# Kernel optimization log

Hardware: AMD Instinct MI355X
Metric: run time of the kernel (lower is better)

## Reference

```python
import jax, jax.numpy as jnp
import numpy as np

B, I, O, C, U = 32, 2048, 32, 16, 32  # batch, in_channels(caps), out_capsules, in_capsules(dim), unit_size
NUM_ITERS = 3


def setup_inputs() -> dict:
    key = jax.random.key(0)
    k1, k2 = jax.random.split(key)
    x = jax.random.normal(k1, (B, I, C), dtype=jnp.float32)
    w = jax.random.normal(k2, (I, O, C, U), dtype=jnp.float32)
    return {"x": x, "w": w}


def _squash(v):
    # faithful to original: vec * |vec| / (1 + |vec|^2), norm over last (unit) dim
    n = jnp.linalg.norm(v, axis=-1, keepdims=True)
    return v * n / (1.0 + n * n)


def reference(x, w):
    # u_hat[b,i,o,u] = sum_c x[b,i,c] * w[i,o,c,u]   (the original's x @ w with singleton dims dropped)
    u_hat = jnp.einsum('bic,iocu->biou', x, w)  # [B,I,O,U]
    b_log = jnp.zeros((I, O, 1), dtype=x.dtype)
    v = None
    for _ in range(NUM_ITERS):
        # original computes softmax over dim=2 of [I,O,1] (a singleton dim) -> all ones; kept faithful
        c = jax.nn.softmax(b_log, axis=2)[..., 0]  # [I,O]
        s = jnp.einsum('io,biou->bou', c, u_hat)   # sum over input capsules
        v = _squash(s)                              # [B,O,U]
        # agreement: per-(b,i,o) dot(u_hat, v), then mean over batch (original's update.mean(dim=0))
        agree = jnp.einsum('biou,bou->io', u_hat, v) / B
        b_log = b_log + agree[..., None]
    return v[:, :, None, :]  # matches original v.squeeze(1) -> [B, O, 1, U]
```

## Files before the change

### kernel.cpp

```cpp
#include <hip/hip_runtime.h>
#include <math.h>

#define B_   32
#define I_   2048
#define O_   32
#define C_   16
#define U_   32
#define NCOL (O_ * U_)
#define TI   4
#define NBLK (I_ / TI)
#define SLICE (B_ * NCOL)


__global__ __launch_bounds__(256, 2) void caps_partial(const float* __restrict__ x,
                                                       const float* __restrict__ w,
                                                       float* __restrict__ ws) {
    __shared__ float xs[TI * C_ * 33];
    const int tid = threadIdx.x;
    const int i0 = blockIdx.x * TI;

    for (int k = tid; k < B_ * TI * C_; k += 256) {
        int b   = k >> 6;
        int rem = k & 63;
        xs[rem * 33 + b] = x[(size_t)b * (I_ * C_) + (size_t)i0 * C_ + rem];
    }
    __syncthreads();

    const int o  = tid >> 3;
    const int u4 = (tid & 7) << 2;
    const float* wp = w + (size_t)i0 * (O_ * C_ * U_) + o * (C_ * U_) + u4;

    float4 acc[B_];
#pragma unroll
    for (int b = 0; b < B_; ++b) acc[b] = make_float4(0.f, 0.f, 0.f, 0.f);

    for (int il = 0; il < TI; ++il) {
        const float* wpi = wp + (size_t)il * (O_ * C_ * U_);
        const float* xr  = &xs[il * C_ * 33];
        float4 wv[C_];
#pragma unroll
        for (int c = 0; c < C_; ++c) wv[c] = *(const float4*)(wpi + c * U_);
#pragma unroll
        for (int c = 0; c < C_; ++c) {
            const float* xc = xr + c * 33;
#pragma unroll
            for (int b = 0; b < B_; ++b) {
                float xb = xc[b];
                acc[b].x = fmaf(xb, wv[c].x, acc[b].x);
                acc[b].y = fmaf(xb, wv[c].y, acc[b].y);
                acc[b].z = fmaf(xb, wv[c].z, acc[b].z);
                acc[b].w = fmaf(xb, wv[c].w, acc[b].w);
            }
        }
    }

    float* op = ws + (size_t)blockIdx.x * SLICE + u4 + o * U_;
#pragma unroll
    for (int b = 0; b < B_; ++b)
        *(float4*)(op + (size_t)b * NCOL) = acc[b];
}

__global__ void caps_reduce_squash(const float* __restrict__ ws,
                                   float* __restrict__ out) {
    int t = blockIdx.x * 256 + threadIdx.x;
    float s = 0.f;
#pragma unroll 8
    for (int p = 0; p < NBLK; ++p)
        s += ws[(size_t)p * SLICE + t];
    float ss = s * s;
    ss += __shfl_xor(ss, 1);
    ss += __shfl_xor(ss, 2);
    ss += __shfl_xor(ss, 4);
    ss += __shfl_xor(ss, 8);
    ss += __shfl_xor(ss, 16);
    float n = sqrtf(ss);
    out[t] = s * n / (1.0f + ss);
}

__global__ __launch_bounds__(256, 2) void caps_main_atomic(const float* __restrict__ x,
                                                           const float* __restrict__ w,
                                                           float* __restrict__ out) {
    __shared__ float xs[TI * C_ * 33];
    const int tid = threadIdx.x;
    const int i0 = blockIdx.x * TI;
    for (int k = tid; k < B_ * TI * C_; k += 256) {
        int b = k >> 6, rem = k & 63;
        xs[rem * 33 + b] = x[(size_t)b * (I_ * C_) + (size_t)i0 * C_ + rem];
    }
    __syncthreads();
    const int o = tid >> 3, u4 = (tid & 7) << 2;
    const float* wp = w + (size_t)i0 * (O_ * C_ * U_) + o * (C_ * U_) + u4;
    float4 acc[B_];
#pragma unroll
    for (int b = 0; b < B_; ++b) acc[b] = make_float4(0.f, 0.f, 0.f, 0.f);
    for (int il = 0; il < TI; ++il) {
        const float* wpi = wp + (size_t)il * (O_ * C_ * U_);
        const float* xr = &xs[il * C_ * 33];
#pragma unroll
        for (int c = 0; c < C_; ++c) {
            float4 wv = *(const float4*)(wpi + c * U_);
            const float* xc = xr + c * 33;
#pragma unroll
            for (int b = 0; b < B_; ++b) {
                float xb = xc[b];
                acc[b].x = fmaf(xb, wv.x, acc[b].x);
                acc[b].y = fmaf(xb, wv.y, acc[b].y);
                acc[b].z = fmaf(xb, wv.z, acc[b].z);
                acc[b].w = fmaf(xb, wv.w, acc[b].w);
            }
        }
    }
    float* op = out + o * U_ + u4;
#pragma unroll
    for (int b = 0; b < B_; ++b) {
        float* p = op + (size_t)b * NCOL;
        atomicAdd(p + 0, acc[b].x);
        atomicAdd(p + 1, acc[b].y);
        atomicAdd(p + 2, acc[b].z);
        atomicAdd(p + 3, acc[b].w);
    }
}

__global__ void caps_squash_inplace(float* __restrict__ out) {
    int t = blockIdx.x * 256 + threadIdx.x;
    float s = out[t];
    float ss = s * s;
    ss += __shfl_xor(ss, 1);
    ss += __shfl_xor(ss, 2);
    ss += __shfl_xor(ss, 4);
    ss += __shfl_xor(ss, 8);
    ss += __shfl_xor(ss, 16);
    float n = sqrtf(ss);
    out[t] = s * n / (1.0f + ss);
}

extern "C" void kernel_launch(void* const* d_in, const int* in_sizes, int n_in,
                              void* d_out, int out_size, void* d_ws, size_t ws_size,
                              hipStream_t stream) {
    const float* x = (const float*)d_in[0];
    const float* w = (const float*)d_in[1];
    float* out = (float*)d_out;

    const size_t need = (size_t)NBLK * SLICE * sizeof(float);
    if (ws_size >= need) {
        float* ws = (float*)d_ws;
        caps_partial<<<NBLK, 256, 0, stream>>>(x, w, ws);
        caps_reduce_squash<<<SLICE / 256, 256, 0, stream>>>(ws, out);
    } else {
        hipMemsetAsync(out, 0, (size_t)SLICE * sizeof(float), stream);
        caps_main_atomic<<<NBLK, 256, 0, stream>>>(x, w, out);
        caps_squash_inplace<<<SLICE / 256, 256, 0, stream>>>(out);
    }
}
```

Before: 223.7 us.

## Split batch across thread halves, vectorize LDS reads, parallelize reduction

The partial kernel now uses 512 threads per block, with each half handling 16 of the 32 batch rows. This halves the accumulator registers per thread so more waves can be resident. Shared-memory x reads become float4 loads with a padded stride of 36, and weights are loaded in groups of four channels instead of all sixteen at once. The reduce kernel splits the 512-partial sum between two thread halves and combines them through shared memory, giving twice as many threads to the memory-bound reduction. The cost is weight loads duplicated across the two halves and possible bank conflicts from the new padding.

After: 211.8 us. -5.4%, faster.

```diff
diff --git a/kernel.cpp b/kernel.cpp
--- a/kernel.cpp
+++ b/kernel.cpp
@@ -10,71 +10,101 @@
 #define TI   4
 #define NBLK (I_ / TI)
 #define SLICE (B_ * NCOL)
+#define BH   16
+#define XS   36
 
 
-__global__ __launch_bounds__(256, 2) void caps_partial(const float* __restrict__ x,
+__global__ __launch_bounds__(512, 4) void caps_partial(const float* __restrict__ x,
                                                        const float* __restrict__ w,
                                                        float* __restrict__ ws) {
-    __shared__ float xs[TI * C_ * 33];
+    __shared__ float xs[TI * C_ * XS];
     const int tid = threadIdx.x;
     const int i0 = blockIdx.x * TI;
 
-    for (int k = tid; k < B_ * TI * C_; k += 256) {
+    for (int k = tid; k < B_ * TI * C_; k += 512) {
         int b   = k >> 6;
         int rem = k & 63;
-        xs[rem * 33 + b] = x[(size_t)b * (I_ * C_) + (size_t)i0 * C_ + rem];
+        xs[rem * XS + b] = x[(size_t)b * (I_ * C_) + (size_t)i0 * C_ + rem];
     }
     __syncthreads();
 
-    const int o  = tid >> 3;
-    const int u4 = (tid & 7) << 2;
+    const int bh = tid >> 8;
+    const int ct = tid & 255;
+    const int o  = ct >> 3;
+    const int u4 = (ct & 7) << 2;
     const float* wp = w + (size_t)i0 * (O_ * C_ * U_) + o * (C_ * U_) + u4;
 
-    float4 acc[B_];
+    float4 acc[BH];
 #pragma unroll
-    for (int b = 0; b < B_; ++b) acc[b] = make_float4(0.f, 0.f, 0.f, 0.f);
+    for (int b = 0; b < BH; ++b) acc[b] = make_float4(0.f, 0.f, 0.f, 0.f);
 
     for (int il = 0; il < TI; ++il) {
         const float* wpi = wp + (size_t)il * (O_ * C_ * U_);
-        const float* xr  = &xs[il * C_ * 33];
-        float4 wv[C_];
+        const float* xr  = &xs[il * C_ * XS + bh * BH];
 #pragma unroll
-        for (int c = 0; c < C_; ++c) wv[c] = *(const float4*)(wpi + c * U_);
+        for (int cc = 0; cc < C_; cc += 4) {
+            float4 wv[4];
 #pragma unroll
-        for (int c = 0; c < C_; ++c) {
-            const float* xc = xr + c * 33;
+            for (int j = 0; j < 4; ++j)
+                wv[j] = *(const float4*)(wpi + (cc + j) * U_);
 #pragma unroll
-            for (int b = 0; b < B_; ++b) {
-                float xb = xc[b];
-                acc[b].x = fmaf(xb, wv[c].x, acc[b].x);
-                acc[b].y = fmaf(xb, wv[c].y, acc[b].y);
-                acc[b].z = fmaf(xb, wv[c].z, acc[b].z);
-                acc[b].w = fmaf(xb, wv[c].w, acc[b].w);
+            for (int j = 0; j < 4; ++j) {
+                const float4* xv = (const float4*)(xr + (cc + j) * XS);
+#pragma unroll
+                for (int q = 0; q < 4; ++q) {
+                    float4 xq = xv[q];
+                    float4* a = &acc[q * 4];
+                    a[0].x = fmaf(xq.x, wv[j].x, a[0].x);
+                    a[0].y = fmaf(xq.x, wv[j].y, a[0].y);
+                    a[0].z = fmaf(xq.x, wv[j].z, a[0].z);
+                    a[0].w = fmaf(xq.x, wv[j].w, a[0].w);
+                    a[1].x = fmaf(xq.y, wv[j].x, a[1].x);
+                    a[1].y = fmaf(xq.y, wv[j].y, a[1].y);
+                    a[1].z = fmaf(xq.y, wv[j].z, a[1].z);
+                    a[1].w = fmaf(xq.y, wv[j].w, a[1].w);
+                    a[2].x = fmaf(xq.z, wv[j].x, a[2].x);
+                    a[2].y = fmaf(xq.z, wv[j].y, a[2].y);
+                    a[2].z = fmaf(xq.z, wv[j].z, a[2].z);
+                    a[2].w = fmaf(xq.z, wv[j].w, a[2].w);
+                    a[3].x = fmaf(xq.w, wv[j].x, a[3].x);
+                    a[3].y = fmaf(xq.w, wv[j].y, a[3].y);
+                    a[3].z = fmaf(xq.w, wv[j].z, a[3].z);
+                    a[3].w = fmaf(xq.w, wv[j].w, a[3].w);
+                }
             }
         }
     }
 
-    float* op = ws + (size_t)blockIdx.x * SLICE + u4 + o * U_;
+    float* op = ws + (size_t)blockIdx.x * SLICE + (size_t)(bh * BH) * NCOL + o * U_ + u4;
 #pragma unroll
-    for (int b = 0; b < B_; ++b)
+    for (int b = 0; b < BH; ++b)
         *(float4*)(op + (size_t)b * NCOL) = acc[b];
 }
 
-__global__ void caps_reduce_squash(const float* __restrict__ ws,
-                                   float* __restrict__ out) {
-    int t = blockIdx.x * 256 + threadIdx.x;
+__global__ __launch_bounds__(256) void caps_reduce_squash(const float* __restrict__ ws,
+                                                          float* __restrict__ out) {
+    __shared__ float sh[128];
+    const int tl = threadIdx.x & 127;
+    const int ph = threadIdx.x >> 7;
+    const int t  = blockIdx.x * 128 + tl;
+    const float* p = ws + (size_t)ph * (NBLK / 2) * SLICE + t;
     float s = 0.f;
-#pragma unroll 8
-    for (int p = 0; p < NBLK; ++p)
-        s += ws[(size_t)p * SLICE + t];
-    float ss = s * s;
-    ss += __shfl_xor(ss, 1);
-    ss += __shfl_xor(ss, 2);
-    ss += __shfl_xor(ss, 4);
-    ss += __shfl_xor(ss, 8);
-    ss += __shfl_xor(ss, 16);
-    float n = sqrtf(ss);
-    out[t] = s * n / (1.0f + ss);
+#pragma unroll 16
+    for (int i = 0; i < NBLK / 2; ++i)
+        s += p[(size_t)i * SLICE];
+    if (ph) sh[tl] = s;
+    __syncthreads();
+    if (ph == 0) {
+        s += sh[tl];
+        float ss = s * s;
+        ss += __shfl_xor(ss, 1);
+        ss += __shfl_xor(ss, 2);
+        ss += __shfl_xor(ss, 4);
+        ss += __shfl_xor(ss, 8);
+        ss += __shfl_xor(ss, 16);
+        float n = sqrtf(ss);
+        out[t] = s * n / (1.0f + ss);
+    }
 }
 
 __global__ __launch_bounds__(256, 2) void caps_main_atomic(const float* __restrict__ x,
@@ -144,11 +174,11 @@
     const size_t need = (size_t)NBLK * SLICE * sizeof(float);
     if (ws_size >= need) {
         float* ws = (float*)d_ws;
-        caps_partial<<<NBLK, 256, 0, stream>>>(x, w, ws);
-        caps_reduce_squash<<<SLICE / 256, 256, 0, stream>>>(ws, out);
+        caps_partial<<<NBLK, 512, 0, stream>>>(x, w, ws);
+        caps_reduce_squash<<<SLICE / 128, 256, 0, stream>>>(ws, out);
     } else {
         hipMemsetAsync(out, 0, (size_t)SLICE * sizeof(float), stream);
-        caps_main_atomic<<<NBLK, 256, 0, stream>>>(x, w, out);
+        caps_main_atomic<<<I_ / TI, 256, 0, stream>>>(x, w, out);
         caps_squash_inplace<<<SLICE / 256, 256, 0, stream>>>(out);
     }
 }
```
